# Optimization experiments

Hardware: AMD Instinct MI355X
Metric: run time of the kernel (lower is better)

## Reference

```python
import jax, jax.numpy as jnp
import numpy as np

B, T, C = 4, 2048, 1024
H = 16
D = C // H  # head_dim = 64


def setup_inputs() -> dict:
    key = jax.random.key(0)
    k1, k2, k3 = jax.random.split(key, 3)
    x = jax.random.normal(k1, (B, T, C), dtype=jnp.float32)
    w_qkv = jax.random.normal(k2, (C, 3 * C), dtype=jnp.float32) * (1.0 / np.sqrt(C))
    b_qkv = jnp.zeros((3 * C,), dtype=jnp.float32)
    w_out = jax.random.normal(k3, (C, C), dtype=jnp.float32) * (1.0 / np.sqrt(C))
    b_out = jnp.zeros((C,), dtype=jnp.float32)
    return {"x": x, "w_qkv": w_qkv, "b_qkv": b_qkv, "w_out": w_out, "b_out": b_out}


def reference(x, w_qkv, b_qkv, w_out, b_out):
    # QKV projection: [B,T,3C]
    qkv = x @ w_qkv + b_qkv
    q, k, v = jnp.split(qkv, 3, axis=-1)
    # [B,H,T,D]
    q = q.reshape(B, T, H, D).transpose(0, 2, 1, 3)
    k = k.reshape(B, T, H, D).transpose(0, 2, 1, 3)
    v = v.reshape(B, T, H, D).transpose(0, 2, 1, 3)
    scale = 1.0 / np.sqrt(D)
    # scores: [B,H,T,T]
    scores = jnp.einsum("bhqd,bhkd->bhqk", q, k) * scale
    causal = jnp.tril(jnp.ones((T, T), dtype=bool))
    scores = jnp.where(causal[None, None, :, :], scores, -jnp.inf)
    attn = jax.nn.softmax(scores, axis=-1)
    out = jnp.einsum("bhqk,bhkd->bhqd", attn, v)
    out = out.transpose(0, 2, 1, 3).reshape(B, T, C)
    return out @ w_out + b_out
```

## Files before the change

### kernel.cpp

```cpp
#include <hip/hip_runtime.h>
#include <hip/hip_bf16.h>

#define BB 4
#define TT 2048
#define CC 1024
#define HH 16
#define DD 64

typedef __attribute__((ext_vector_type(8))) short short8;
typedef __attribute__((ext_vector_type(4))) float f32x4;

__device__ __forceinline__ float bf2f(short s) {
  unsigned u = ((unsigned)(unsigned short)s) << 16;
  float f;
  __builtin_memcpy(&f, &u, 4);
  return f;
}
__device__ __forceinline__ short f2bf(float f) {
  unsigned u;
  __builtin_memcpy(&u, &f, 4);
  u = (u + 0x7fffu + ((u >> 16) & 1u)) >> 16;
  return (short)u;
}

__device__ __forceinline__ unsigned cvt_pk_bf16(float lo, float hi) {
  unsigned r;
  asm("v_cvt_pk_bf16_f32 %0, %1, %2" : "=v"(r) : "v"(lo), "v"(hi));
  return r;
}

__device__ __forceinline__ float exp2_fast(float x) {
  float r;
  asm("v_exp_f32 %0, %1" : "=v"(r) : "v"(x));
  return r;
}

template <int CTRL>
__device__ __forceinline__ float dpp_f(float v) {
  union { float f; int i; } u;
  u.f = v;
  u.i = __builtin_amdgcn_update_dpp(0, u.i, CTRL, 0xf, 0xf, true);
  return u.f;
}
__device__ __forceinline__ float rowmax16(float v) {
  v = fmaxf(v, dpp_f<0x128>(v));
  v = fmaxf(v, dpp_f<0x124>(v));
  v = fmaxf(v, dpp_f<0x4E>(v));
  v = fmaxf(v, dpp_f<0xB1>(v));
  return v;
}
__device__ __forceinline__ float rowsum16(float v) {
  v += dpp_f<0x128>(v);
  v += dpp_f<0x124>(v);
  v += dpp_f<0x4E>(v);
  v += dpp_f<0xB1>(v);
  return v;
}

__device__ __forceinline__ void gload_lds16(const void* g, void* l) {
  __builtin_amdgcn_global_load_lds(
      (const __attribute__((address_space(1))) void*)g,
      (__attribute__((address_space(3))) void*)l, 16, 0, 0);
}

__global__ __launch_bounds__(256) void cast_bf16_kernel(
    const float* __restrict__ in, short* __restrict__ out, int n) {
  int i = (blockIdx.x * 256 + threadIdx.x) * 4;
  if (i >= n) return;
  float4 v = *(const float4*)&in[i];
  short4 o;
  o.x = f2bf(v.x); o.y = f2bf(v.y); o.z = f2bf(v.z); o.w = f2bf(v.w);
  *(short4*)&out[i] = o;
}

__global__ __launch_bounds__(256) void transpose_cast_kernel(
    const float* __restrict__ in, short* __restrict__ out, int R, int Cc) {
  __shared__ float tile[32][33];
  const int tx = threadIdx.x, ty = threadIdx.y;
  const int c0 = blockIdx.x * 32, r0 = blockIdx.y * 32;
#pragma unroll
  for (int i = 0; i < 32; i += 8)
    tile[ty + i][tx] = in[(size_t)(r0 + ty + i) * Cc + c0 + tx];
  __syncthreads();
#pragma unroll
  for (int i = 0; i < 32; i += 8)
    out[(size_t)(c0 + ty + i) * R + r0 + tx] = f2bf(tile[tx][ty + i]);
}

__global__ __launch_bounds__(256) void v_transpose_kernel(
    const short* __restrict__ vb, short* __restrict__ vt) {
  __shared__ int tile[32][33];
  const int tx = threadIdx.x, ty = threadIdx.y;
  const int bh = blockIdx.z;
  const int d0 = blockIdx.x * 32, t0 = blockIdx.y * 32;
  const short* src = vb + (size_t)bh * TT * DD;
  short* dstp = vt + (size_t)bh * DD * TT;
#pragma unroll
  for (int i = 0; i < 32; i += 8)
    tile[ty + i][tx] = src[(size_t)(t0 + ty + i) * DD + d0 + tx];
  __syncthreads();
#pragma unroll
  for (int i = 0; i < 32; i += 8)
    dstp[(size_t)(d0 + ty + i) * TT + t0 + tx] = (short)tile[tx][ty + i];
}

template <int MODE>
__global__ __launch_bounds__(256) void gemm_bf16(
    const short* __restrict__ A, const short* __restrict__ Bt,
    const float* __restrict__ bias, float* __restrict__ outF,
    short* __restrict__ outQ, short* __restrict__ outK, short* __restrict__ outV,
    int M, int N, int K) {
  __shared__ __align__(16) short As[128 * 32];
  __shared__ __align__(16) short Bs[128 * 32];
  const int tid = threadIdx.x;
  const int lane = tid & 63, wid = tid >> 6;
  const int wm = wid >> 1, wn = wid & 1;
  const int row0 = blockIdx.y * 128, col0 = blockIdx.x * 128;
  const int fr = lane & 15, fq = lane >> 4;
  const short* Ab = A + (size_t)row0 * K;
  const short* Bb = Bt + (size_t)col0 * K;
  const int sr = tid >> 2;
  const int so = (tid & 3) * 8;

  f32x4 acc[4][4];
#pragma unroll
  for (int m = 0; m < 4; ++m)
#pragma unroll
    for (int n = 0; n < 4; ++n) {
      f32x4 z = {0.f, 0.f, 0.f, 0.f};
      acc[m][n] = z;
    }

  for (int k0 = 0; k0 < K; k0 += 32) {
    __syncthreads();
    gload_lds16(Ab + (size_t)sr * K + k0 + so, &As[tid * 8]);
    gload_lds16(Ab + (size_t)(sr + 64) * K + k0 + so, &As[2048 + tid * 8]);
    gload_lds16(Bb + (size_t)sr * K + k0 + so, &Bs[tid * 8]);
    gload_lds16(Bb + (size_t)(sr + 64) * K + k0 + so, &Bs[2048 + tid * 8]);
    __syncthreads();
    short8 a[4], b[4];
#pragma unroll
    for (int m = 0; m < 4; ++m)
      a[m] = *(const short8*)&As[(wm * 64 + m * 16 + fr) * 32 + fq * 8];
#pragma unroll
    for (int n = 0; n < 4; ++n)
      b[n] = *(const short8*)&Bs[(wn * 64 + n * 16 + fr) * 32 + fq * 8];
#pragma unroll
    for (int m = 0; m < 4; ++m)
#pragma unroll
      for (int n = 0; n < 4; ++n)
        acc[m][n] = __builtin_amdgcn_mfma_f32_16x16x32_bf16(a[m], b[n], acc[m][n], 0, 0, 0);
  }

  float bv[4];
#pragma unroll
  for (int n = 0; n < 4; ++n) bv[n] = bias[col0 + wn * 64 + n * 16 + fr];

  if (MODE == 0) {
#pragma unroll
    for (int m = 0; m < 4; ++m) {
      const int grow = row0 + wm * 64 + m * 16 + fq * 4;
#pragma unroll
      for (int n = 0; n < 4; ++n) {
        const int gcol = col0 + wn * 64 + n * 16 + fr;
#pragma unroll
        for (int r = 0; r < 4; ++r)
          outF[(size_t)(grow + r) * N + gcol] = acc[m][n][r] + bv[n];
      }
    }
  } else {
#pragma unroll
    for (int n = 0; n < 4; ++n) {
      const int gcol = col0 + wn * 64 + n * 16 + fr;
      const int which = gcol >> 10;
      const int h = (gcol & 1023) >> 6;
      const int d = gcol & 63;
      short* dst = (which == 0) ? outQ : (which == 1) ? outK : outV;
#pragma unroll
      for (int m = 0; m < 4; ++m) {
        const int grow = row0 + wm * 64 + m * 16 + fq * 4;
#pragma unroll
        for (int r = 0; r < 4; ++r) {
          const int gb = (grow + r) >> 11;
          const int gt = (grow + r) & 2047;
          const int bh = gb * HH + h;
          dst[((size_t)bh * TT + gt) * DD + d] = f2bf(acc[m][n][r] + bv[n]);
        }
      }
    }
  }
}

#define C2 0.18033688f

__global__ __launch_bounds__(256) void attn_mfma_kernel(
    const short* __restrict__ q,
    const short* __restrict__ k,
    const short* __restrict__ vt,
    short* __restrict__ ctx) {
  __shared__ __align__(16) short Ks[2][128 * 64];
  __shared__ __align__(16) short Vs[2][64 * 128];
  __shared__ __align__(16) short Ps[4][32 * 64];
  const int tid = threadIdx.x, lane = tid & 63, wid = tid >> 6;
  const int fr = lane & 15, fq = lane >> 4;
  const int lin = blockIdx.x;
  const int bh = lin & 63;
  const int qt = 15 - (lin >> 6);
  const int q0 = qt * 128;
  const int qw0 = q0 + wid * 32;
  const short* kbp = k + (size_t)bh * TT * DD;
  const short* vbp = vt + (size_t)bh * DD * TT;
  char* PsB = (char*)&Ps[wid][0];

#define KSB(c) ((char*)&Ks[0][0] + (c) * (128 * 64 * 2))
#define VSB(c) ((char*)&Vs[0][0] + (c) * (64 * 128 * 2))

  short8 aq[2][2];
#pragma unroll
  for (int m = 0; m < 2; ++m)
#pragma unroll
    for (int ks = 0; ks < 2; ++ks)
      aq[m][ks] = *(const short8*)&q[((size_t)bh * TT + qw0 + m * 16 + fr) * DD + ks * 32 + fq * 8];

  float M[2][4], L[2][4];
  f32x4 o[2][4];
#pragma unroll
  for (int m = 0; m < 2; ++m)
#pragma unroll
    for (int r = 0; r < 4; ++r) { M[m][r] = -1e30f; L[m][r] = 0.f; }
#pragma unroll
  for (int m = 0; m < 2; ++m)
#pragma unroll
    for (int dg = 0; dg < 4; ++dg) {
      f32x4 z = {0.f, 0.f, 0.f, 0.f};
      o[m][dg] = z;
    }

  const int nt = qt + 1;

#define STAGE(c, tt)                                                           \
  do {                                                                         \
    const int kv0_ = (tt) * 128;                                               \
    _Pragma("unroll") for (int b_ = 0; b_ < 4; ++b_) {                         \
      const int lo_ = b_ * 4096 + tid * 16;                                    \
      const int row_ = lo_ >> 7;                                               \
      const int colb_ = lo_ & 127;                                             \
      const int src_ = colb_ ^ ((row_ & 7) << 4);                              \
      gload_lds16(kbp + ((size_t)(kv0_ + row_)) * DD + (src_ >> 1),            \
                  KSB(c) + lo_);                                               \
    }                                                                          \
    _Pragma("unroll") for (int b_ = 0; b_ < 4; ++b_) {                         \
      const int lo_ = b_ * 4096 + tid * 16;                                    \
      const int row_ = lo_ >> 8;                                               \
      const int colb_ = lo_ & 255;                                             \
      const int src_ = colb_ ^ ((row_ & 7) << 4);                              \
      gload_lds16(vbp + (size_t)row_ * TT + kv0_ + (src_ >> 1),                \
                  VSB(c) + lo_);                                               \
    }                                                                          \
  } while (0)

  STAGE(0, 0);

  for (int t = 0; t < nt; ++t) {
    const int cur = t & 1;
    asm volatile("s_waitcnt vmcnt(0)" ::: "memory");
    __builtin_amdgcn_s_barrier();
    if (t + 1 < nt) STAGE(cur ^ 1, t + 1);
    const int kv0 = t * 128;
    if (kv0 > qw0 + 31) continue;

#pragma unroll
    for (int sub = 0; sub < 2; ++sub) {
      const int kv0s = kv0 + sub * 64;
      if (kv0s > qw0 + 31) continue;
      const bool domask = (kv0s + 63 > qw0);

      short8 bk[4][2];
#pragma unroll
      for (int n = 0; n < 4; ++n) {
        const int row = sub * 64 + n * 16 + fr;
#pragma unroll
        for (int ks = 0; ks < 2; ++ks)
          bk[n][ks] = *(const short8*)(KSB(cur) + row * 128 +
                                       (((ks * 64 + fq * 16) ^ ((row & 7) << 4))));
      }
      f32x4 s[2][4];
      __builtin_amdgcn_s_setprio(1);
#pragma unroll
      for (int m = 0; m < 2; ++m)
#pragma unroll
        for (int n = 0; n < 4; ++n) {
          f32x4 z = {0.f, 0.f, 0.f, 0.f};
          s[m][n] = z;
#pragma unroll
          for (int ks = 0; ks < 2; ++ks)
            s[m][n] = __builtin_amdgcn_mfma_f32_16x16x32_bf16(aq[m][ks], bk[n][ks], s[m][n], 0, 0, 0);
        }
      __builtin_amdgcn_s_setprio(0);

      if (domask) {
#pragma unroll
        for (int m = 0; m < 2; ++m)
#pragma unroll
          for (int n = 0; n < 4; ++n)
#pragma unroll
            for (int r = 0; r < 4; ++r) {
              const int qq = qw0 + m * 16 + fq * 4 + r;
              const int kk = kv0s + n * 16 + fr;
              if (kk > qq) s[m][n][r] = -1e30f;
            }
      }

#pragma unroll
      for (int m = 0; m < 2; ++m) {
        float rm2[4];
#pragma unroll
        for (int r = 0; r < 4; ++r) {
          float rm = fmaxf(fmaxf(s[m][0][r], s[m][1][r]), fmaxf(s[m][2][r], s[m][3][r]));
          rm2[r] = rowmax16(rm) * C2;
        }
        float dmax = fmaxf(fmaxf(rm2[0] - M[m][0], rm2[1] - M[m][1]),
                           fmaxf(rm2[2] - M[m][2], rm2[3] - M[m][3]));
        if (__any(dmax > 8.0f)) {
#pragma unroll
          for (int r = 0; r < 4; ++r) {
            const float Mn = fmaxf(M[m][r], rm2[r]);
            const float corr = exp2_fast(M[m][r] - Mn);
            M[m][r] = Mn;
            L[m][r] *= corr;
#pragma unroll
            for (int dg = 0; dg < 4; ++dg) o[m][dg][r] *= corr;
          }
        }
        float psum[4] = {0.f, 0.f, 0.f, 0.f};
        const int brow = m * 16 + fq * 4;
        unsigned short* pw = (unsigned short*)PsB;
#pragma unroll
        for (int n = 0; n < 4; ++n) {
          const float p0 = exp2_fast(__builtin_fmaf(s[m][n][0], C2, -M[m][0]));
          const float p1 = exp2_fast(__builtin_fmaf(s[m][n][1], C2, -M[m][1]));
          const float p2 = exp2_fast(__builtin_fmaf(s[m][n][2], C2, -M[m][2]));
          const float p3 = exp2_fast(__builtin_fmaf(s[m][n][3], C2, -M[m][3]));
          psum[0] += p0; psum[1] += p1; psum[2] += p2; psum[3] += p3;
          const unsigned u0 = cvt_pk_bf16(p0, p1);
          const unsigned u1 = cvt_pk_bf16(p2, p3);
          const int colb = n * 32 + fr * 2;
          pw[((brow + 0) * 128 + (colb ^ (((brow + 0) & 7) << 4))) >> 1] = (unsigned short)u0;
          pw[((brow + 1) * 128 + (colb ^ (((brow + 1) & 7) << 4))) >> 1] = (unsigned short)(u0 >> 16);
          pw[((brow + 2) * 128 + (colb ^ (((brow + 2) & 7) << 4))) >> 1] = (unsigned short)u1;
          pw[((brow + 3) * 128 + (colb ^ (((brow + 3) & 7) << 4))) >> 1] = (unsigned short)(u1 >> 16);
        }
#pragma unroll
        for (int r = 0; r < 4; ++r) L[m][r] += rowsum16(psum[r]);
      }

      short8 ap[2][2], bv[4][2];
#pragma unroll
      for (int m = 0; m < 2; ++m) {
        const int qrow = m * 16 + fr;
#pragma unroll
        for (int ks = 0; ks < 2; ++ks)
          ap[m][ks] = *(const short8*)(PsB + qrow * 128 +
                                       (((ks * 64 + fq * 16) ^ ((qrow & 7) << 4))));
      }
#pragma unroll
      for (int dg = 0; dg < 4; ++dg) {
        const int row = dg * 16 + fr;
#pragma unroll
        for (int ks = 0; ks < 2; ++ks)
          bv[dg][ks] = *(const short8*)(VSB(cur) + row * 256 +
                                        (((sub * 128 + ks * 64 + fq * 16) ^ ((row & 7) << 4))));
      }
      __builtin_amdgcn_s_setprio(1);
#pragma unroll
      for (int m = 0; m < 2; ++m)
#pragma unroll
        for (int dg = 0; dg < 4; ++dg)
#pragma unroll
          for (int ks = 0; ks < 2; ++ks)
            o[m][dg] = __builtin_amdgcn_mfma_f32_16x16x32_bf16(ap[m][ks], bv[dg][ks], o[m][dg], 0, 0, 0);
      __builtin_amdgcn_s_setprio(0);
    }
  }

  const int b = bh >> 4, h = bh & 15;
#pragma unroll
  for (int m = 0; m < 2; ++m)
#pragma unroll
    for (int dg = 0; dg < 4; ++dg)
#pragma unroll
      for (int r = 0; r < 4; ++r) {
        const int qq = qw0 + m * 16 + fq * 4 + r;
        ctx[((size_t)(b * TT + qq)) * CC + h * DD + dg * 16 + fr] =
            f2bf(o[m][dg][r] / L[m][r]);
      }
}

extern "C" void kernel_launch(void* const* d_in, const int* in_sizes, int n_in,
                              void* d_out, int out_size, void* d_ws, size_t ws_size,
                              hipStream_t stream) {
  (void)in_sizes; (void)n_in; (void)out_size; (void)ws_size;
  const float* x = (const float*)d_in[0];
  const float* w_qkv = (const float*)d_in[1];
  const float* b_qkv = (const float*)d_in[2];
  const float* w_out = (const float*)d_in[3];
  const float* b_out = (const float*)d_in[4];
  float* out = (float*)d_out;

  char* w = (char*)d_ws;
  short* xb    = (short*)w; w += (size_t)BB * TT * CC * 2;
  short* wqkvT = (short*)w; w += (size_t)3 * CC * CC * 2;
  short* woutT = (short*)w; w += (size_t)CC * CC * 2;
  short* qb    = (short*)w; w += (size_t)BB * HH * TT * DD * 2;
  short* kb    = (short*)w; w += (size_t)BB * HH * TT * DD * 2;
  short* vtb   = (short*)w; w += (size_t)BB * HH * DD * TT * 2;
  short* ctx   = (short*)w; w += (size_t)BB * TT * CC * 2;

  const int M = BB * TT;

  cast_bf16_kernel<<<dim3((M * CC) / 4 / 256), dim3(256), 0, stream>>>(x, xb, M * CC);
  transpose_cast_kernel<<<dim3(3 * CC / 32, CC / 32), dim3(32, 8), 0, stream>>>(
      w_qkv, wqkvT, CC, 3 * CC);
  transpose_cast_kernel<<<dim3(CC / 32, CC / 32), dim3(32, 8), 0, stream>>>(
      w_out, woutT, CC, CC);

  gemm_bf16<1><<<dim3((3 * CC) / 128, M / 128), dim3(256), 0, stream>>>(
      xb, wqkvT, b_qkv, nullptr, qb, kb, ctx, M, 3 * CC, CC);

  v_transpose_kernel<<<dim3(DD / 32, TT / 32, BB * HH), dim3(32, 8), 0, stream>>>(
      ctx, vtb);

  attn_mfma_kernel<<<dim3(16 * 64), dim3(256), 0, stream>>>(qb, kb, vtb, ctx);

  gemm_bf16<0><<<dim3(CC / 128, M / 128), dim3(256), 0, stream>>>(
      ctx, woutT, b_out, out, nullptr, nullptr, nullptr, M, CC, CC);
}
```

Before: 296.6 us.

## Double-buffer GEMM LDS tiles and remap workgroups across XCDs

The bf16 GEMM now keeps two LDS stages, so the global-to-LDS load for the next K tile is issued before the MFMAs on the current tile, and each iteration needs one barrier instead of two. The grid becomes 1D, and block IDs are remapped so consecutive tiles land on the same XCD, which should improve L2 reuse of the A and B panels. MFMA sections get raised wave priority via s_setprio. LDS use doubles per block, which may lower occupancy. The remap assumes the workgroup count is divisible by 8.

```diff
diff --git a/kernel.cpp b/kernel.cpp
--- a/kernel.cpp
+++ b/kernel.cpp
@@ -110,12 +110,17 @@
     const float* __restrict__ bias, float* __restrict__ outF,
     short* __restrict__ outQ, short* __restrict__ outK, short* __restrict__ outV,
     int M, int N, int K) {
-  __shared__ __align__(16) short As[128 * 32];
-  __shared__ __align__(16) short Bs[128 * 32];
+  __shared__ __align__(16) short As[2][128 * 32];
+  __shared__ __align__(16) short Bs[2][128 * 32];
   const int tid = threadIdx.x;
   const int lane = tid & 63, wid = tid >> 6;
   const int wm = wid >> 1, wn = wid & 1;
-  const int row0 = blockIdx.y * 128, col0 = blockIdx.x * 128;
+  const int nbx = N >> 7;
+  const int nwg = nbx * (M >> 7);
+  const int lin0 = blockIdx.x;
+  const int lin = (lin0 & 7) * (nwg >> 3) + (lin0 >> 3);
+  const int bx = lin % nbx, by = lin / nbx;
+  const int row0 = by * 128, col0 = bx * 128;
   const int fr = lane & 15, fq = lane >> 4;
   const short* Ab = A + (size_t)row0 * K;
   const short* Bb = Bt + (size_t)col0 * K;
@@ -131,25 +136,35 @@
       acc[m][n] = z;
     }
 
-  for (int k0 = 0; k0 < K; k0 += 32) {
-    __syncthreads();
-    gload_lds16(Ab + (size_t)sr * K + k0 + so, &As[tid * 8]);
-    gload_lds16(Ab + (size_t)(sr + 64) * K + k0 + so, &As[2048 + tid * 8]);
-    gload_lds16(Bb + (size_t)sr * K + k0 + so, &Bs[tid * 8]);
-    gload_lds16(Bb + (size_t)(sr + 64) * K + k0 + so, &Bs[2048 + tid * 8]);
-    __syncthreads();
+#define GSTAGE(c, k0)                                                          \
+  do {                                                                         \
+    gload_lds16(Ab + (size_t)sr * K + (k0) + so, &As[c][tid * 8]);             \
+    gload_lds16(Ab + (size_t)(sr + 64) * K + (k0) + so, &As[c][2048 + tid * 8]); \
+    gload_lds16(Bb + (size_t)sr * K + (k0) + so, &Bs[c][tid * 8]);             \
+    gload_lds16(Bb + (size_t)(sr + 64) * K + (k0) + so, &Bs[c][2048 + tid * 8]); \
+  } while (0)
+
+  GSTAGE(0, 0);
+  const int nkt = K >> 5;
+  for (int kt = 0; kt < nkt; ++kt) {
+    const int cur = kt & 1;
+    asm volatile("s_waitcnt vmcnt(0)" ::: "memory");
+    __builtin_amdgcn_s_barrier();
+    if (kt + 1 < nkt) GSTAGE(cur ^ 1, (kt + 1) * 32);
     short8 a[4], b[4];
 #pragma unroll
     for (int m = 0; m < 4; ++m)
-      a[m] = *(const short8*)&As[(wm * 64 + m * 16 + fr) * 32 + fq * 8];
+      a[m] = *(const short8*)&As[cur][(wm * 64 + m * 16 + fr) * 32 + fq * 8];
 #pragma unroll
     for (int n = 0; n < 4; ++n)
-      b[n] = *(const short8*)&Bs[(wn * 64 + n * 16 + fr) * 32 + fq * 8];
+      b[n] = *(const short8*)&Bs[cur][(wn * 64 + n * 16 + fr) * 32 + fq * 8];
+    __builtin_amdgcn_s_setprio(1);
 #pragma unroll
     for (int m = 0; m < 4; ++m)
 #pragma unroll
       for (int n = 0; n < 4; ++n)
         acc[m][n] = __builtin_amdgcn_mfma_f32_16x16x32_bf16(a[m], b[n], acc[m][n], 0, 0, 0);
+    __builtin_amdgcn_s_setprio(0);
   }
 
   float bv[4];
@@ -424,7 +439,7 @@
   transpose_cast_kernel<<<dim3(CC / 32, CC / 32), dim3(32, 8), 0, stream>>>(
       w_out, woutT, CC, CC);
 
-  gemm_bf16<1><<<dim3((3 * CC) / 128, M / 128), dim3(256), 0, stream>>>(
+  gemm_bf16<1><<<dim3((3 * CC / 128) * (M / 128)), dim3(256), 0, stream>>>(
       xb, wqkvT, b_qkv, nullptr, qb, kb, ctx, M, 3 * CC, CC);
 
   v_transpose_kernel<<<dim3(DD / 32, TT / 32, BB * HH), dim3(32, 8), 0, stream>>>(
@@ -432,6 +447,6 @@
 
   attn_mfma_kernel<<<dim3(16 * 64), dim3(256), 0, stream>>>(qb, kb, vtb, ctx);
 
-  gemm_bf16<0><<<dim3(CC / 128, M / 128), dim3(256), 0, stream>>>(
+  gemm_bf16<0><<<dim3((CC / 128) * (M / 128)), dim3(256), 0, stream>>>(
       ctx, woutT, b_out, out, nullptr, nullptr, nullptr, M, CC, CC);
 }
```

After: 287.8 us. 1.03x faster.
